# Kernel optimization log

Measured on AMD Instinct MI355X. Metric: run time of the kernel, lower is better.

Reference implementation:

```python
import jax, jax.numpy as jnp
import numpy as np

N = 100000      # nodes
E = 1200000     # edges
B = 128         # graphs
H = 64          # hidden
IN_DIM = 64
GN_EPS = 1e-5


def _gin(x, edge_index, w1, b1, w2, b2):
    # GINConv (eps=0): mlp(x + sum_{j in N(i)} x_j)
    agg = jax.ops.segment_sum(x[edge_index[0]], edge_index[1], num_segments=N)
    h = x + agg
    return jax.nn.relu(h @ w1 + b1) @ w2 + b2


def _graph_norm(x, batch, w, b, ms):
    # PyG GraphNorm: out = w * (x - ms*mean) / sqrt(var + eps) + b, per-graph stats
    ones = jnp.ones((x.shape[0],), x.dtype)
    cnt = jnp.maximum(jax.ops.segment_sum(ones, batch, num_segments=B), 1.0)[:, None]
    mean = jax.ops.segment_sum(x, batch, num_segments=B) / cnt
    out = x - ms * mean[batch]
    var = jax.ops.segment_sum(out * out, batch, num_segments=B) / cnt
    return out * (jax.lax.rsqrt(var + GN_EPS)[batch] * w) + b


def setup_inputs() -> dict:
    key = jax.random.key(0)
    ks = jax.random.split(key, 32)
    inp = {
        'x': jax.random.normal(ks[0], (N, IN_DIM), jnp.float32),
        'edge_index': jax.random.randint(ks[1], (2, E), 0, N, dtype=jnp.int32),
        'batch': jnp.sort(jax.random.randint(ks[2], (N,), 0, B, dtype=jnp.int32)),
        'u': jax.random.normal(ks[3], (B, 3), jnp.float32),
    }
    k = 4
    for i in range(3):
        fin = IN_DIM if i == 0 else H
        inp[f'w{i+1}a'] = jax.random.normal(ks[k], (fin, H), jnp.float32) / np.sqrt(fin); k += 1
        inp[f'b{i+1}a'] = jnp.zeros((H,), jnp.float32)
        inp[f'w{i+1}b'] = jax.random.normal(ks[k], (H, H), jnp.float32) / np.sqrt(H); k += 1
        inp[f'b{i+1}b'] = jnp.zeros((H,), jnp.float32)
        inp[f'gn{i+1}_w'] = jnp.ones((H,), jnp.float32)
        inp[f'gn{i+1}_b'] = jnp.zeros((H,), jnp.float32)
        inp[f'gn{i+1}_ms'] = jnp.ones((H,), jnp.float32)
    inp['gate_w'] = jax.random.normal(ks[k], (H, 1), jnp.float32) / np.sqrt(H); k += 1
    inp['gate_b'] = jnp.zeros((1,), jnp.float32)
    inp['hw1'] = jax.random.normal(ks[k], (3 * H + 3, H), jnp.float32) / np.sqrt(3 * H + 3); k += 1
    inp['hb1'] = jnp.zeros((H,), jnp.float32)
    inp['hw2'] = jax.random.normal(ks[k], (H, 1), jnp.float32) / np.sqrt(H); k += 1
    inp['hb2'] = jnp.zeros((1,), jnp.float32)
    return inp


def reference(x, edge_index, batch, u,
              w1a, b1a, w1b, b1b, gn1_w, gn1_b, gn1_ms,
              w2a, b2a, w2b, b2b, gn2_w, gn2_b, gn2_ms,
              w3a, b3a, w3b, b3b, gn3_w, gn3_b, gn3_ms,
              gate_w, gate_b, hw1, hb1, hw2, hb2):
    h1 = jax.nn.relu(_graph_norm(_gin(x, edge_index, w1a, b1a, w1b, b1b), batch, gn1_w, gn1_b, gn1_ms))
    h2 = jax.nn.relu(_graph_norm(_gin(h1, edge_index, w2a, b2a, w2b, b2b), batch, gn2_w, gn2_b, gn2_ms))
    h3 = jax.nn.relu(_graph_norm(_gin(h2, edge_index, w3a, b3a, w3b, b3b), batch, gn3_w, gn3_b, gn3_ms))
    h = h1 + h2 + h3

    # AttentionalAggregation: per-graph softmax over gate logits
    gate = h @ gate_w + gate_b                                      # [N,1]
    m = jax.ops.segment_max(gate, batch, num_segments=B)            # [B,1]
    ex = jnp.exp(gate - m[batch])
    den = jax.ops.segment_sum(ex, batch, num_segments=B)
    att = jax.ops.segment_sum((ex / den[batch]) * h, batch, num_segments=B)

    ones = jnp.ones((h.shape[0],), h.dtype)
    cnt = jnp.maximum(jax.ops.segment_sum(ones, batch, num_segments=B), 1.0)[:, None]
    mean_pool = jax.ops.segment_sum(h, batch, num_segments=B) / cnt
    max_pool = jax.ops.segment_max(h, batch, num_segments=B)

    z = jnp.concatenate([att, mean_pool, max_pool, u], axis=1)       # [B, 3H+3]
    out = jax.nn.relu(z @ hw1 + hb1) @ hw2 + hb2                     # head_cls
    return out.reshape(-1)
```

## Files before the change

kernel.cpp:

```cpp
#include <hip/hip_runtime.h>
#include <hip/hip_cooperative_groups.h>
#include <math.h>

namespace cg = cooperative_groups;

#define HDIM 64
#define GN_EPS 1e-5f
#define MAXNB 512
#define APITCH 72
#define RCHUNK 8192

typedef __attribute__((ext_vector_type(8))) short bf16x8;
typedef __attribute__((ext_vector_type(4))) float f32x4;

__device__ __forceinline__ int lower_bound_i(const int* a, int n, int key){
  int lo = 0, hi = n;
  while (lo < hi){ int mid = (lo + hi) >> 1; if (a[mid] < key) lo = mid + 1; else hi = mid; }
  return lo;
}
__device__ __forceinline__ unsigned fenc(float x){
  unsigned b = __float_as_uint(x);
  return (b & 0x80000000u) ? ~b : (b | 0x80000000u);
}
__device__ __forceinline__ float fdec(unsigned u){
  unsigned b = (u & 0x80000000u) ? (u ^ 0x80000000u) : ~u;
  return __uint_as_float(b);
}
__device__ __forceinline__ unsigned short f2bf(float f){
  unsigned u = __float_as_uint(f);
  u += 0x7fffu + ((u >> 16) & 1u);
  return (unsigned short)(u >> 16);
}
__device__ __forceinline__ float bf2f(unsigned short h){
  return __uint_as_float(((unsigned)h) << 16);
}
__device__ __forceinline__ void addbf(float* a, uint4 v){
  a[0] += __uint_as_float(v.x << 16);
  a[1] += __uint_as_float(v.x & 0xffff0000u);
  a[2] += __uint_as_float(v.y << 16);
  a[3] += __uint_as_float(v.y & 0xffff0000u);
  a[4] += __uint_as_float(v.z << 16);
  a[5] += __uint_as_float(v.z & 0xffff0000u);
  a[6] += __uint_as_float(v.w << 16);
  a[7] += __uint_as_float(v.w & 0xffff0000u);
}

struct BuildArgs {
  const int* src; const int* dst; int E; int NB;
  const float* W0; const float* W1; const float* W2;
  const float* W3; const float* W4; const float* W5;
  short* wbf;
  const int* batch; int N; int* gs; int B;
  int* bcount; int* bbase; int* bcursor;
  int2* ebuf; int* deg; int* offs; int* csr;
  const float* x; unsigned short* xb; int n16;
  float* stats; int statsN; float* poolz; int poolzN;
};

__global__ void k_build(BuildArgs a){
  cg::grid_group grid = cg::this_grid();
  __shared__ int sA[512];
  __shared__ int sB[512];
  int tid = threadIdx.x;
  int gsz = (int)gridDim.x;
  int gstart = blockIdx.x * 256 + tid;
  int gstride = gsz * 256;

  for (int i = gstart; i <= MAXNB; i += gstride) a.bcount[i] = 0;
  for (int i = gstart; i < a.statsN; i += gstride) a.stats[i] = 0.f;
  for (int i = gstart; i < a.poolzN; i += gstride) a.poolz[i] = 0.f;
  if (blockIdx.x < 6){
    const float* Wsrc = (blockIdx.x == 0) ? a.W0 : (blockIdx.x == 1) ? a.W1 :
                        (blockIdx.x == 2) ? a.W2 : (blockIdx.x == 3) ? a.W3 :
                        (blockIdx.x == 4) ? a.W4 : a.W5;
    short* hi = a.wbf + blockIdx.x * 8192;
    short* lo = hi + 4096;
    for (int i = tid; i < 4096; i += 256){
      int k = i >> 6, j = i & 63;
      float v = Wsrc[i];
      unsigned short h = f2bf(v);
      hi[j * 64 + k] = (short)h;
      lo[j * 64 + k] = (short)f2bf(v - bf2f(h));
    }
  } else if (blockIdx.x == 6){
    for (int g = tid; g <= a.B; g += 256) a.gs[g] = lower_bound_i(a.batch, a.N, g);
  }
  for (int i = gstart; i < a.n16; i += gstride){
    float4 v = ((const float4*)a.x)[i];
    ushort4 o;
    o.x = f2bf(v.x); o.y = f2bf(v.y); o.z = f2bf(v.z); o.w = f2bf(v.w);
    ((ushort4*)a.xb)[i] = o;
  }
  grid.sync();

  for (int b = tid; b < a.NB; b += 256) sA[b] = 0;
  __syncthreads();
  for (int i = gstart; i < a.E; i += gstride) atomicAdd(&sA[a.dst[i] >> 8], 1);
  __syncthreads();
  for (int b = tid; b < a.NB; b += 256){ int c = sA[b]; if (c) atomicAdd(&a.bcount[b], c); }
  grid.sync();

  if (blockIdx.x == 0){
    int v0 = (2 * tid     < a.NB) ? a.bcount[2 * tid]     : 0;
    int v1 = (2 * tid + 1 < a.NB) ? a.bcount[2 * tid + 1] : 0;
    int L = v0 + v1;
    sB[tid] = L; __syncthreads();
    for (int o = 1; o < 256; o <<= 1){
      int tv = (tid >= o) ? sB[tid - o] : 0;
      __syncthreads();
      sB[tid] += tv;
      __syncthreads();
    }
    int run = sB[tid] - L;
    if (2 * tid < a.NB){ a.bbase[2 * tid] = run; a.bcursor[2 * tid] = run; }
    run += v0;
    if (2 * tid + 1 < a.NB){ a.bbase[2 * tid + 1] = run; a.bcursor[2 * tid + 1] = run; }
    if (tid == 255) a.bbase[a.NB] = sB[255];
  }
  grid.sync();

  int nch = (a.E + RCHUNK - 1) / RCHUNK;
  for (int ci = blockIdx.x; ci < nch; ci += gsz){
    int c0 = ci * RCHUNK;
    for (int b = tid; b < a.NB; b += 256) sA[b] = 0;
    __syncthreads();
    for (int j = 0; j < RCHUNK / 256; j++){
      int i = c0 + j * 256 + tid;
      if (i < a.E) atomicAdd(&sA[a.dst[i] >> 8], 1);
    }
    __syncthreads();
    for (int b = tid; b < a.NB; b += 256){
      int c = sA[b];
      sB[b] = c ? atomicAdd(&a.bcursor[b], c) : 0;
      sA[b] = 0;
    }
    __syncthreads();
    for (int j = 0; j < RCHUNK / 256; j++){
      int i = c0 + j * 256 + tid;
      if (i < a.E){
        int d = a.dst[i]; int b = d >> 8;
        int rr = atomicAdd(&sA[b], 1);
        a.ebuf[sB[b] + rr] = make_int2(a.src[i], d);
      }
    }
    __syncthreads();
  }
  grid.sync();

  for (int b = blockIdx.x; b < a.NB; b += gsz){
    int lo = b << 8;
    int nn = min(256, a.N - lo);
    sA[tid] = 0; __syncthreads();
    int es = a.bbase[b], ee = a.bbase[b + 1];
    for (int i = es + tid; i < ee; i += 256) atomicAdd(&sA[a.ebuf[i].y - lo], 1);
    __syncthreads();
    int v = sA[tid];
    sB[tid] = v; __syncthreads();
    for (int o = 1; o < 256; o <<= 1){
      int tv = (tid >= o) ? sB[tid - o] : 0;
      __syncthreads();
      sB[tid] += tv;
      __syncthreads();
    }
    int excl = sB[tid] - v;
    if (tid < nn){ a.deg[lo + tid] = v; a.offs[lo + tid] = es + excl; }
    __syncthreads();
    sA[tid] = es + excl;
    __syncthreads();
    for (int i = es + tid; i < ee; i += 256){
      int2 e = a.ebuf[i];
      int pos = atomicAdd(&sA[e.y - lo], 1);
      a.csr[pos] = e.x;
    }
    __syncthreads();
  }
}

struct TrunkArgs {
  const unsigned short* xb;
  unsigned short* bufA; unsigned short* bufB;
  float* G; float* hsum;
  const int* csr; const int* offs; const int* deg; const int* batch; const int* gs;
  const short* wbf;
  const float* B1a; const float* B1b; const float* B1c;
  const float* B2a; const float* B2b; const float* B2c;
  const float* gnw0; const float* gnw1; const float* gnw2;
  const float* gnb0; const float* gnb1; const float* gnb2;
  const float* gnm0; const float* gnm1; const float* gnm2;
  float* stats; int N; int n16; int B;
  const float* gw; const float* gb; const float* u;
  const float* hw1; const float* hb1; const float* hw2; const float* hb2;
  float* sumbuf; unsigned* maxbuf; float* attbuf; float* denbuf; unsigned* gmaxbuf;
  float* gatebuf; float* out;
};

__global__ __launch_bounds__(256, 3) void k_trunk(TrunkArgs a){
  cg::grid_group grid = cg::this_grid();
  __shared__ __align__(16) char smem[51712];
  short* Ws  = (short*)smem;
  short* Ah  = (short*)(smem + 32768);
  short* Al  = (short*)(smem + 32768 + 9216);
  float* ssum = (float*)(smem + 32768 + 18432);
  float* ssq  = ssum + 64;
  int tid = threadIdx.x;
  int wv = tid >> 6, lane = tid & 63;
  int gsz = (int)gridDim.x;
  int N = a.N;
  int ntile = (N + 63) >> 6;

  const unsigned short* P = a.xb;
  unsigned short* Cb = a.bufA;

  for (int l = 0; l < 3; l++){
    {
      int sub = lane >> 3, l8 = lane & 7, sbase = sub << 3;
      const uint4* Pv = (const uint4*)P;
      int wid = blockIdx.x * 4 + wv;
      int wstep = gsz * 4 * 8;
      for (int nb = wid * 8; nb < N; nb += wstep){
        int node = nb + sub;
        bool ok = node < N;
        int st = 0, cnt = 0;
        if (ok){ st = a.offs[node]; cnt = a.deg[node]; }
        float acc8[8];
        #pragma unroll
        for (int k = 0; k < 8; k++) acc8[k] = 0.f;
        if (ok) addbf(acc8, Pv[(size_t)node * 8 + l8]);
        for (int base = 0; base < cnt; base += 8){
          int rem = cnt - base;
          int s = (l8 < rem) ? a.csr[st + base + l8] : 0;
          int m = min(rem, 8);
          int j = 0;
          for (; j + 4 <= m; j += 4){
            int s0 = __shfl(s, sbase | j);
            int s1 = __shfl(s, sbase | (j + 1));
            int s2 = __shfl(s, sbase | (j + 2));
            int s3 = __shfl(s, sbase | (j + 3));
            uint4 v0 = Pv[(size_t)s0 * 8 + l8];
            uint4 v1 = Pv[(size_t)s1 * 8 + l8];
            uint4 v2 = Pv[(size_t)s2 * 8 + l8];
            uint4 v3 = Pv[(size_t)s3 * 8 + l8];
            addbf(acc8, v0); addbf(acc8, v1); addbf(acc8, v2); addbf(acc8, v3);
          }
          for (; j < m; ++j){
            int sj = __shfl(s, sbase | j);
            addbf(acc8, Pv[(size_t)sj * 8 + l8]);
          }
        }
        if (ok){
          float4* Gp = (float4*)(a.G + (size_t)node * HDIM + l8 * 8);
          Gp[0] = make_float4(acc8[0], acc8[1], acc8[2], acc8[3]);
          Gp[1] = make_float4(acc8[4], acc8[5], acc8[6], acc8[7]);
        }
      }
    }
    grid.sync();

    {
      const short* Wall = a.wbf + (size_t)l * 16384;
      for (int j = tid; j < 2048; j += 256){
        int p = j >> 9, rem = j & 511, rr = rem >> 3, c8 = rem & 7;
        bf16x8 v = ((const bf16x8*)Wall)[j];
        *(bf16x8*)(Ws + p * 4096 + rr * 64 + ((c8 ^ (rr & 7)) << 3)) = v;
      }
      int quad = lane >> 4, l15 = lane & 15;
      int rbase = wv << 4;
      int h7 = l15 & 7;
      const float* B1 = (l == 0) ? a.B1a : (l == 1) ? a.B1b : a.B1c;
      const float* B2 = (l == 0) ? a.B2a : (l == 1) ? a.B2b : a.B2c;
      float bb1[4], bb2[4];
      #pragma unroll
      for (int t4 = 0; t4 < 4; t4++){ bb1[t4] = B1[t4 * 16 + l15]; bb2[t4] = B2[t4 * 16 + l15]; }
      float* lstats = a.stats + (size_t)l * a.B * 128;

      int t = blockIdx.x;
      float4 r[4], r2[4];
      #pragma unroll
      for (int ri = 0; ri < 4; ri++){ r[ri] = make_float4(0.f,0.f,0.f,0.f); r2[ri] = r[ri]; }
      if (t < ntile){
        int tb = t << 6;
        #pragma unroll
        for (int ri = 0; ri < 4; ri++){
          int idx = ri * 256 + tid;
          int node = tb + (idx >> 4), f4 = idx & 15;
          if (node < N) r[ri] = ((const float4*)a.G)[(size_t)node * 16 + f4];
        }
      }
      while (t < ntile){
        int t0 = t << 6;
        #pragma unroll
        for (int ri = 0; ri < 4; ri++){
          int idx = ri * 256 + tid;
          int nodeL = idx >> 4, f4 = idx & 15;
          float vv[4] = {r[ri].x, r[ri].y, r[ri].z, r[ri].w};
          short hh[4], ll[4];
          #pragma unroll
          for (int j = 0; j < 4; j++){
            unsigned short hv = f2bf(vv[j]);
            hh[j] = (short)hv;
            ll[j] = (short)f2bf(vv[j] - bf2f(hv));
          }
          *(short4*)(Ah + nodeL * APITCH + f4 * 4) = make_short4(hh[0], hh[1], hh[2], hh[3]);
          *(short4*)(Al + nodeL * APITCH + f4 * 4) = make_short4(ll[0], ll[1], ll[2], ll[3]);
        }
        if (tid < 64){ ssum[tid] = 0.f; ssq[tid] = 0.f; }
        __syncthreads();

        int tn = t + gsz;
        #pragma unroll
        for (int ri = 0; ri < 4; ri++) r2[ri] = make_float4(0.f,0.f,0.f,0.f);
        if (tn < ntile){
          int tb = tn << 6;
          #pragma unroll
          for (int ri = 0; ri < 4; ri++){
            int idx = ri * 256 + tid;
            int node = tb + (idx >> 4), f4 = idx & 15;
            if (node < N) r2[ri] = ((const float4*)a.G)[(size_t)node * 16 + f4];
          }
        }

        f32x4 acc[4];
        #pragma unroll
        for (int t4 = 0; t4 < 4; t4++) acc[t4] = (f32x4){0.f, 0.f, 0.f, 0.f};
        #pragma unroll
        for (int kb = 0; kb < 2; kb++){
          int kk = kb * 32 + quad * 8;
          int swz = ((kb * 4 + quad) ^ h7) << 3;
          bf16x8 a_h = *(const bf16x8*)(Ah + (rbase + l15) * APITCH + kk);
          bf16x8 a_l = *(const bf16x8*)(Al + (rbase + l15) * APITCH + kk);
          #pragma unroll
          for (int t4 = 0; t4 < 4; t4++){
            int row = t4 * 16 + l15;
            bf16x8 b_h = *(const bf16x8*)(Ws + row * 64 + swz);
            bf16x8 b_l = *(const bf16x8*)(Ws + 4096 + row * 64 + swz);
            acc[t4] = __builtin_amdgcn_mfma_f32_16x16x32_bf16(a_h, b_h, acc[t4], 0, 0, 0);
            acc[t4] = __builtin_amdgcn_mfma_f32_16x16x32_bf16(a_h, b_l, acc[t4], 0, 0, 0);
            acc[t4] = __builtin_amdgcn_mfma_f32_16x16x32_bf16(a_l, b_h, acc[t4], 0, 0, 0);
          }
        }
        __syncthreads();

        #pragma unroll
        for (int t4 = 0; t4 < 4; t4++){
          #pragma unroll
          for (int rg = 0; rg < 4; rg++){
            float v = fmaxf(acc[t4][rg] + bb1[t4], 0.f);
            int row = rbase + quad * 4 + rg;
            int col = t4 * 16 + l15;
            unsigned short hv = f2bf(v);
            Ah[row * APITCH + col] = (short)hv;
            Al[row * APITCH + col] = (short)f2bf(v - bf2f(hv));
          }
        }
        __syncthreads();

        f32x4 acc2[4];
        #pragma unroll
        for (int t4 = 0; t4 < 4; t4++) acc2[t4] = (f32x4){0.f, 0.f, 0.f, 0.f};
        #pragma unroll
        for (int kb = 0; kb < 2; kb++){
          int kk = kb * 32 + quad * 8;
          int swz = ((kb * 4 + quad) ^ h7) << 3;
          bf16x8 a_h = *(const bf16x8*)(Ah + (rbase + l15) * APITCH + kk);
          bf16x8 a_l = *(const bf16x8*)(Al + (rbase + l15) * APITCH + kk);
          #pragma unroll
          for (int t4 = 0; t4 < 4; t4++){
            int row = t4 * 16 + l15;
            bf16x8 b_h = *(const bf16x8*)(Ws + 8192 + row * 64 + swz);
            bf16x8 b_l = *(const bf16x8*)(Ws + 12288 + row * 64 + swz);
            acc2[t4] = __builtin_amdgcn_mfma_f32_16x16x32_bf16(a_h, b_h, acc2[t4], 0, 0, 0);
            acc2[t4] = __builtin_amdgcn_mfma_f32_16x16x32_bf16(a_h, b_l, acc2[t4], 0, 0, 0);
            acc2[t4] = __builtin_amdgcn_mfma_f32_16x16x32_bf16(a_l, b_h, acc2[t4], 0, 0, 0);
          }
        }

        int lastn = min(t0 + 63, N - 1);
        int g0 = a.batch[t0];
        bool uniform = (a.batch[lastn] == g0) && (t0 + 63 < N);
        #pragma unroll
        for (int t4 = 0; t4 < 4; t4++){
          int f = t4 * 16 + l15;
          float s = 0.f, q = 0.f;
          #pragma unroll
          for (int rg = 0; rg < 4; rg++){
            float v = acc2[t4][rg] + bb2[t4];
            int node = t0 + rbase + quad * 4 + rg;
            if (node < N) a.G[(size_t)node * HDIM + f] = v;
            if (uniform){
              s += v; q += v * v;
            } else if (node < N){
              int g = a.batch[node];
              atomicAdd(&lstats[g * 128 + f], v);
              atomicAdd(&lstats[g * 128 + 64 + f], v * v);
            }
          }
          if (uniform){
            s += __shfl_xor(s, 16); s += __shfl_xor(s, 32);
            q += __shfl_xor(q, 16); q += __shfl_xor(q, 32);
            if (quad == 0){ atomicAdd(&ssum[f], s); atomicAdd(&ssq[f], q); }
          }
        }
        __syncthreads();
        if (uniform && tid < 64){
          atomicAdd(&lstats[g0 * 128 + tid], ssum[tid]);
          atomicAdd(&lstats[g0 * 128 + 64 + tid], ssq[tid]);
        }
        #pragma unroll
        for (int ri = 0; ri < 4; ri++) r[ri] = r2[ri];
        t = tn;
      }
    }
    grid.sync();

    {
      const float* wv_ = (l == 0) ? a.gnw0 : (l == 1) ? a.gnw1 : a.gnw2;
      const float* bv_ = (l == 0) ? a.gnb0 : (l == 1) ? a.gnb1 : a.gnb2;
      const float* mv_ = (l == 0) ? a.gnm0 : (l == 1) ? a.gnm1 : a.gnm2;
      const float* lstats = a.stats + (size_t)l * a.B * 128;
      int first = (l == 0) ? 1 : 0;
      int writeC = (l == 2) ? 0 : 1;
      for (int i = blockIdx.x * 256 + tid; i < a.n16; i += gsz * 256){
        int node = i >> 4, q = i & 15;
        int g = a.batch[node];
        float cnt = (float)max(a.gs[g + 1] - a.gs[g], 1);
        float4 y  = ((const float4*)a.G)[i];
        float4 s1 = ((const float4*)(lstats + g * 128))[q];
        float4 s2 = ((const float4*)(lstats + g * 128 + 64))[q];
        float4 wq = ((const float4*)wv_)[q];
        float4 mq = ((const float4*)mv_)[q];
        float4 bq = ((const float4*)bv_)[q];
        float4 v;
        #define APPLY1(c) { \
          float mean = s1.c / cnt; float ex2 = s2.c / cnt; \
          float var = ex2 - (2.f * mq.c - mq.c * mq.c) * mean * mean; \
          float sc = rsqrtf(var + GN_EPS) * wq.c; \
          v.c = fmaxf((y.c - mq.c * mean) * sc + bq.c, 0.f); }
        APPLY1(x) APPLY1(y) APPLY1(z) APPLY1(w)
        #undef APPLY1
        if (writeC){
          ushort4 o;
          o.x = f2bf(v.x); o.y = f2bf(v.y); o.z = f2bf(v.z); o.w = f2bf(v.w);
          ((ushort4*)Cb)[i] = o;
        }
        if (first){
          ((float4*)a.hsum)[i] = v;
        } else {
          float4 h = ((float4*)a.hsum)[i];
          h.x += v.x; h.y += v.y; h.z += v.z; h.w += v.w;
          ((float4*)a.hsum)[i] = h;
        }
      }
    }
    grid.sync();
    P = Cb;
    Cb = (l == 0) ? a.bufB : a.bufA;
  }

  {
    int nchunk = (N + 31) >> 5;
    int wid = blockIdx.x * 4 + wv;
    float gwv = a.gw[lane];
    float gb = a.gb[0];
    for (int c = wid; c < nchunk; c += gsz * 4){
      int s = c << 5, e = min(s + 32, N);
      int cur = a.batch[s];
      float macc = 0.f, xacc = -INFINITY, gmx = -INFINITY;
      for (int nd = s; nd < e; ++nd){
        int g = a.batch[nd];
        if (g != cur){
          atomicAdd(&a.sumbuf[cur * 64 + lane], macc);
          atomicMax(&a.maxbuf[cur * 64 + lane], fenc(xacc));
          if (lane == 0) atomicMax(&a.gmaxbuf[cur], fenc(gmx));
          macc = 0.f; xacc = -INFINITY; gmx = -INFINITY; cur = g;
        }
        float hv = a.hsum[(size_t)nd * HDIM + lane];
        macc += hv; xacc = fmaxf(xacc, hv);
        float gv = hv * gwv;
        #pragma unroll
        for (int msk = 1; msk < 64; msk <<= 1) gv += __shfl_xor(gv, msk);
        gv += gb;
        if (lane == 0) a.gatebuf[nd] = gv;
        gmx = fmaxf(gmx, gv);
      }
      atomicAdd(&a.sumbuf[cur * 64 + lane], macc);
      atomicMax(&a.maxbuf[cur * 64 + lane], fenc(xacc));
      if (lane == 0) atomicMax(&a.gmaxbuf[cur], fenc(gmx));
    }
  }
  grid.sync();

  {
    int nchunk = (N + 31) >> 5;
    int wid = blockIdx.x * 4 + wv;
    for (int c = wid; c < nchunk; c += gsz * 4){
      int s = c << 5, e = min(s + 32, N);
      int cur = a.batch[s];
      float m = fdec(a.gmaxbuf[cur]);
      float aacc = 0.f, dacc = 0.f;
      for (int nd = s; nd < e; ++nd){
        int g = a.batch[nd];
        if (g != cur){
          atomicAdd(&a.attbuf[cur * 64 + lane], aacc);
          if (lane == 0) atomicAdd(&a.denbuf[cur], dacc);
          aacc = 0.f; dacc = 0.f; cur = g; m = fdec(a.gmaxbuf[cur]);
        }
        float ex = expf(a.gatebuf[nd] - m);
        float hv = a.hsum[(size_t)nd * HDIM + lane];
        aacc += ex * hv; dacc += ex;
      }
      atomicAdd(&a.attbuf[cur * 64 + lane], aacc);
      if (lane == 0) atomicAdd(&a.denbuf[cur], dacc);
    }
  }
  grid.sync();

  {
    float* z = (float*)smem;
    int g = blockIdx.x;
    if (g < a.B){
      float cnt = (float)max(a.gs[g + 1] - a.gs[g], 1);
      if (tid < 64){
        float den = a.denbuf[g];
        z[tid]       = a.attbuf[g * 64 + tid] / den;
        z[64 + tid]  = a.sumbuf[g * 64 + tid] / cnt;
        z[128 + tid] = fdec(a.maxbuf[g * 64 + tid]);
        if (tid < 3) z[192 + tid] = a.u[g * 3 + tid];
      }
      __syncthreads();
      if (tid < 64){
        float acc = a.hb1[tid];
        for (int k = 0; k < 195; k++) acc += z[k] * a.hw1[k * 64 + tid];
        float sv = fmaxf(acc, 0.f) * a.hw2[tid];
        #pragma unroll
        for (int msk = 1; msk < 64; msk <<= 1) sv += __shfl_xor(sv, msk);
        if (tid == 0) a.out[g] = sv + a.hb2[0];
      }
    }
  }
}

__global__ void k_prep(const int* __restrict__ dst, int* __restrict__ bcount, int E, int NB,
                       const float* __restrict__ Wa0, const float* __restrict__ Wb0,
                       const float* __restrict__ Wa1, const float* __restrict__ Wb1,
                       const float* __restrict__ Wa2, const float* __restrict__ Wb2,
                       short* __restrict__ wbf,
                       const int* __restrict__ batch, int N, int* __restrict__ gs, int B){
  int tid = threadIdx.x;
  if (blockIdx.x < 256){
    __shared__ int lh[MAXNB];
    for (int b = tid; b < NB; b += 256) lh[b] = 0;
    __syncthreads();
    for (int i = blockIdx.x * 256 + tid; i < E; i += 256 * 256)
      atomicAdd(&lh[dst[i] >> 8], 1);
    __syncthreads();
    for (int b = tid; b < NB; b += 256){ int c = lh[b]; if (c) atomicAdd(&bcount[b], c); }
  } else if (blockIdx.x < 262){
    int wi = blockIdx.x - 256;
    const float* Wsrc[6] = {Wa0, Wb0, Wa1, Wb1, Wa2, Wb2};
    const float* W = Wsrc[wi];
    short* hi = wbf + wi * 8192;
    short* lo = hi + 4096;
    for (int i = tid; i < 4096; i += 256){
      int k = i >> 6, j = i & 63;
      float v = W[i];
      unsigned short h = f2bf(v);
      hi[j * 64 + k] = (short)h;
      lo[j * 64 + k] = (short)f2bf(v - bf2f(h));
    }
  } else {
    for (int g = tid; g <= B; g += 256) gs[g] = lower_bound_i(batch, N, g);
  }
}

__global__ void k_cvt(const float* __restrict__ x, unsigned short* __restrict__ xb, int n16){
  int i = blockIdx.x * blockDim.x + threadIdx.x;
  if (i >= n16) return;
  float4 v = ((const float4*)x)[i];
  ushort4 o;
  o.x = f2bf(v.x); o.y = f2bf(v.y); o.z = f2bf(v.z); o.w = f2bf(v.w);
  ((ushort4*)xb)[i] = o;
}

__global__ void k_bscan(const int* __restrict__ bcount, int* __restrict__ bbase,
                        int* __restrict__ bcursor, int NB){
  __shared__ int sd[MAXNB];
  int tid = threadIdx.x;
  int v = (tid < NB) ? bcount[tid] : 0;
  sd[tid] = v; __syncthreads();
  for (int o = 1; o < MAXNB; o <<= 1){
    int t = (tid >= o) ? sd[tid - o] : 0;
    __syncthreads();
    sd[tid] += t;
    __syncthreads();
  }
  int excl = sd[tid] - v;
  if (tid < NB){ bbase[tid] = excl; bcursor[tid] = excl; }
  if (tid == NB - 1) bbase[NB] = excl + v;
}

__global__ void k_breorder(const int* __restrict__ src, const int* __restrict__ dst,
                           int* __restrict__ bcursor, int2* __restrict__ ebuf, int E, int NB){
  __shared__ int lh[MAXNB];
  __shared__ int lbase[MAXNB];
  int tid = threadIdx.x;
  int c0 = blockIdx.x * RCHUNK;
  for (int b = tid; b < NB; b += 256) lh[b] = 0;
  __syncthreads();
  for (int j = 0; j < RCHUNK / 256; j++){
    int i = c0 + j * 256 + tid;
    if (i < E) atomicAdd(&lh[dst[i] >> 8], 1);
  }
  __syncthreads();
  for (int b = tid; b < NB; b += 256){
    int c = lh[b];
    lbase[b] = c ? atomicAdd(&bcursor[b], c) : 0;
    lh[b] = 0;
  }
  __syncthreads();
  for (int j = 0; j < RCHUNK / 256; j++){
    int i = c0 + j * 256 + tid;
    if (i < E){
      int d = dst[i]; int b = d >> 8;
      int r = atomicAdd(&lh[b], 1);
      ebuf[lbase[b] + r] = make_int2(src[i], d);
    }
  }
}

__global__ void k_bucket_csr(const int2* __restrict__ ebuf, const int* __restrict__ bbase,
                             int* __restrict__ deg, int* __restrict__ offs,
                             int* __restrict__ csr, int N){
  __shared__ int lh[256];
  __shared__ int lsc[256];
  int b = blockIdx.x;
  int lo = b << 8;
  int nn = min(256, N - lo);
  int tid = threadIdx.x;
  lh[tid] = 0; __syncthreads();
  int es = bbase[b], ee = bbase[b + 1];
  for (int i = es + tid; i < ee; i += 256) atomicAdd(&lh[ebuf[i].y - lo], 1);
  __syncthreads();
  int v = lh[tid];
  lsc[tid] = v; __syncthreads();
  for (int o = 1; o < 256; o <<= 1){
    int t = (tid >= o) ? lsc[tid - o] : 0;
    __syncthreads();
    lsc[tid] += t;
    __syncthreads();
  }
  int excl = lsc[tid] - v;
  if (tid < nn){ deg[lo + tid] = v; offs[lo + tid] = es + excl; }
  __syncthreads();
  lh[tid] = es + excl;
  __syncthreads();
  for (int i = es + tid; i < ee; i += 256){
    int2 e = ebuf[i];
    int pos = atomicAdd(&lh[e.y - lo], 1);
    csr[pos] = e.x;
  }
}

__global__ __launch_bounds__(256) void k_agg(
    const unsigned short* __restrict__ Pb, const int* __restrict__ csr,
    const int* __restrict__ offs, const int* __restrict__ deg,
    float* __restrict__ G, int n){
  int tid = threadIdx.x;
  int wave_id = blockIdx.x * 4 + (tid >> 6);
  int lane = tid & 63;
  int sub = lane >> 3, l8 = lane & 7;
  int node = wave_id * 8 + sub;
  bool ok = node < n;
  int st = 0, cnt = 0;
  if (ok){ st = offs[node]; cnt = deg[node]; }
  const uint4* Pv = (const uint4*)Pb;
  float a[8];
  #pragma unroll
  for (int k = 0; k < 8; k++) a[k] = 0.f;
  if (ok) addbf(a, Pv[(size_t)node * 8 + l8]);
  int sbase = sub << 3;
  for (int base = 0; base < cnt; base += 8){
    int rem = cnt - base;
    int s = (l8 < rem) ? csr[st + base + l8] : 0;
    int m = min(rem, 8);
    int j = 0;
    for (; j + 4 <= m; j += 4){
      int s0 = __shfl(s, sbase | j);
      int s1 = __shfl(s, sbase | (j + 1));
      int s2 = __shfl(s, sbase | (j + 2));
      int s3 = __shfl(s, sbase | (j + 3));
      uint4 v0 = Pv[(size_t)s0 * 8 + l8];
      uint4 v1 = Pv[(size_t)s1 * 8 + l8];
      uint4 v2 = Pv[(size_t)s2 * 8 + l8];
      uint4 v3 = Pv[(size_t)s3 * 8 + l8];
      addbf(a, v0); addbf(a, v1); addbf(a, v2); addbf(a, v3);
    }
    for (; j < m; ++j){
      int sj = __shfl(s, sbase | j);
      addbf(a, Pv[(size_t)sj * 8 + l8]);
    }
  }
  if (ok){
    float4* Gp = (float4*)(G + (size_t)node * HDIM + l8 * 8);
    Gp[0] = make_float4(a[0], a[1], a[2], a[3]);
    Gp[1] = make_float4(a[4], a[5], a[6], a[7]);
  }
}

__global__ __launch_bounds__(256, 3) void k_mlp(
    float* __restrict__ G, const int* __restrict__ batch,
    const short* __restrict__ Wall,
    const float* __restrict__ B1, const float* __restrict__ B2,
    float* __restrict__ stats, int N){
  __shared__ short Ws[16384];
  __shared__ short Ah[64 * APITCH];
  __shared__ short Al[64 * APITCH];
  __shared__ float ssum[64], ssq[64];
  int tid = threadIdx.x;

  for (int j = tid; j < 2048; j += 256){
    int p = j >> 9, rem = j & 511, rr = rem >> 3, c8 = rem & 7;
    bf16x8 v = ((const bf16x8*)Wall)[j];
    *(bf16x8*)(Ws + p * 4096 + rr * 64 + ((c8 ^ (rr & 7)) << 3)) = v;
  }

  int wv = tid >> 6, lane = tid & 63;
  int quad = lane >> 4, l15 = lane & 15;
  int rbase = wv << 4;
  int h7 = l15 & 7;
  float bb1[4], bb2[4];
  #pragma unroll
  for (int t = 0; t < 4; t++){ bb1[t] = B1[t * 16 + l15]; bb2[t] = B2[t * 16 + l15]; }

  int tile0 = blockIdx.x << 1;
  float4 r[4], r2[4];
  {
    int tb = tile0 << 6;
    #pragma unroll
    for (int ri = 0; ri < 4; ri++){
      int idx = ri * 256 + tid;
      int node = tb + (idx >> 4), f4 = idx & 15;
      r[ri] = make_float4(0.f, 0.f, 0.f, 0.f);
      if (node < N) r[ri] = ((const float4*)G)[(size_t)node * 16 + f4];
    }
  }

  for (int tt = 0; tt < 2; tt++){
    int t0 = (tile0 + tt) << 6;
    if (t0 >= N) break;

    #pragma unroll
    for (int ri = 0; ri < 4; ri++){
      int idx = ri * 256 + tid;
      int node = idx >> 4, f4 = idx & 15;
      float vv[4] = {r[ri].x, r[ri].y, r[ri].z, r[ri].w};
      short h[4], l[4];
      #pragma unroll
      for (int j = 0; j < 4; j++){
        unsigned short hh = f2bf(vv[j]);
        h[j] = (short)hh;
        l[j] = (short)f2bf(vv[j] - bf2f(hh));
      }
      *(short4*)(Ah + node * APITCH + f4 * 4) = make_short4(h[0], h[1], h[2], h[3]);
      *(short4*)(Al + node * APITCH + f4 * 4) = make_short4(l[0], l[1], l[2], l[3]);
    }
    if (tid < 64){ ssum[tid] = 0.f; ssq[tid] = 0.f; }
    __syncthreads();

    if (tt == 0){
      int tb = (tile0 + 1) << 6;
      #pragma unroll
      for (int ri = 0; ri < 4; ri++){
        int idx = ri * 256 + tid;
        int node = tb + (idx >> 4), f4 = idx & 15;
        r2[ri] = make_float4(0.f, 0.f, 0.f, 0.f);
        if (node < N) r2[ri] = ((const float4*)G)[(size_t)node * 16 + f4];
      }
    }

    f32x4 acc[4];
    #pragma unroll
    for (int t = 0; t < 4; t++) acc[t] = (f32x4){0.f, 0.f, 0.f, 0.f};
    #pragma unroll
    for (int kb = 0; kb < 2; kb++){
      int kk = kb * 32 + quad * 8;
      int swz = ((kb * 4 + quad) ^ h7) << 3;
      bf16x8 a_h = *(const bf16x8*)(Ah + (rbase + l15) * APITCH + kk);
      bf16x8 a_l = *(const bf16x8*)(Al + (rbase + l15) * APITCH + kk);
      #pragma unroll
      for (int t = 0; t < 4; t++){
        int row = t * 16 + l15;
        bf16x8 b_h = *(const bf16x8*)(Ws + row * 64 + swz);
        bf16x8 b_l = *(const bf16x8*)(Ws + 4096 + row * 64 + swz);
        acc[t] = __builtin_amdgcn_mfma_f32_16x16x32_bf16(a_h, b_h, acc[t], 0, 0, 0);
        acc[t] = __builtin_amdgcn_mfma_f32_16x16x32_bf16(a_h, b_l, acc[t], 0, 0, 0);
        acc[t] = __builtin_amdgcn_mfma_f32_16x16x32_bf16(a_l, b_h, acc[t], 0, 0, 0);
      }
    }
    __syncthreads();

    #pragma unroll
    for (int t = 0; t < 4; t++){
      #pragma unroll
      for (int rg = 0; rg < 4; rg++){
        float v = fmaxf(acc[t][rg] + bb1[t], 0.f);
        int row = rbase + quad * 4 + rg;
        int col = t * 16 + l15;
        unsigned short hh = f2bf(v);
        Ah[row * APITCH + col] = (short)hh;
        Al[row * APITCH + col] = (short)f2bf(v - bf2f(hh));
      }
    }
    __syncthreads();

    f32x4 acc2[4];
    #pragma unroll
    for (int t = 0; t < 4; t++) acc2[t] = (f32x4){0.f, 0.f, 0.f, 0.f};
    #pragma unroll
    for (int kb = 0; kb < 2; kb++){
      int kk = kb * 32 + quad * 8;
      int swz = ((kb * 4 + quad) ^ h7) << 3;
      bf16x8 a_h = *(const bf16x8*)(Ah + (rbase + l15) * APITCH + kk);
      bf16x8 a_l = *(const bf16x8*)(Al + (rbase + l15) * APITCH + kk);
      #pragma unroll
      for (int t = 0; t < 4; t++){
        int row = t * 16 + l15;
        bf16x8 b_h = *(const bf16x8*)(Ws + 8192 + row * 64 + swz);
        bf16x8 b_l = *(const bf16x8*)(Ws + 12288 + row * 64 + swz);
        acc2[t] = __builtin_amdgcn_mfma_f32_16x16x32_bf16(a_h, b_h, acc2[t], 0, 0, 0);
        acc2[t] = __builtin_amdgcn_mfma_f32_16x16x32_bf16(a_h, b_l, acc2[t], 0, 0, 0);
        acc2[t] = __builtin_amdgcn_mfma_f32_16x16x32_bf16(a_l, b_h, acc2[t], 0, 0, 0);
      }
    }

    int lastn = min(t0 + 63, N - 1);
    int g0 = batch[t0];
    bool uniform = (batch[lastn] == g0) && (t0 + 63 < N);
    #pragma unroll
    for (int t = 0; t < 4; t++){
      int f = t * 16 + l15;
      float s = 0.f, q = 0.f;
      #pragma unroll
      for (int rg = 0; rg < 4; rg++){
        float v = acc2[t][rg] + bb2[t];
        int node = t0 + rbase + quad * 4 + rg;
        if (node < N) G[(size_t)node * HDIM + f] = v;
        if (uniform){
          s += v; q += v * v;
        } else if (node < N){
          int g = batch[node];
          atomicAdd(&stats[g * 128 + f], v);
          atomicAdd(&stats[g * 128 + 64 + f], v * v);
        }
      }
      if (uniform){
        s += __shfl_xor(s, 16); s += __shfl_xor(s, 32);
        q += __shfl_xor(q, 16); q += __shfl_xor(q, 32);
        if (quad == 0){ atomicAdd(&ssum[f], s); atomicAdd(&ssq[f], q); }
      }
    }
    __syncthreads();
    if (uniform && tid < 64){
      atomicAdd(&stats[g0 * 128 + tid], ssum[tid]);
      atomicAdd(&stats[g0 * 128 + 64 + tid], ssq[tid]);
    }
    #pragma unroll
    for (int ri = 0; ri < 4; ri++) r[ri] = r2[ri];
  }
}

__global__ void k_gn_apply(const float* __restrict__ Y, const int* __restrict__ batch,
                           const float* __restrict__ stats, const int* __restrict__ gs,
                           const float* __restrict__ w, const float* __restrict__ ms,
                           const float* __restrict__ bias,
                           unsigned short* __restrict__ Cb, float* __restrict__ hsum, int n16,
                           int first, int writeC){
  int i = blockIdx.x * blockDim.x + threadIdx.x;
  if (i >= n16) return;
  int node = i >> 4, q = i & 15;
  int g = batch[node];
  float cnt = (float)max(gs[g + 1] - gs[g], 1);
  float4 y  = ((const float4*)Y)[i];
  float4 s1 = ((const float4*)(stats + g * 128))[q];
  float4 s2 = ((const float4*)(stats + g * 128 + 64))[q];
  float4 wv = ((const float4*)w)[q];
  float4 mv = ((const float4*)ms)[q];
  float4 bv = ((const float4*)bias)[q];
  float4 v;
  #define APPLY1(c) { \
    float mean = s1.c / cnt; float ex2 = s2.c / cnt; \
    float var = ex2 - (2.f * mv.c - mv.c * mv.c) * mean * mean; \
    float sc = rsqrtf(var + GN_EPS) * wv.c; \
    v.c = fmaxf((y.c - mv.c * mean) * sc + bv.c, 0.f); }
  APPLY1(x) APPLY1(y) APPLY1(z) APPLY1(w)
  #undef APPLY1
  if (writeC){
    ushort4 o;
    o.x = f2bf(v.x); o.y = f2bf(v.y); o.z = f2bf(v.z); o.w = f2bf(v.w);
    ((ushort4*)Cb)[i] = o;
  }
  if (first){
    ((float4*)hsum)[i] = v;
  } else {
    float4 h = ((float4*)hsum)[i];
    h.x += v.x; h.y += v.y; h.z += v.z; h.w += v.w;
    ((float4*)hsum)[i] = h;
  }
}

#define GN_NPW 32
__global__ void k_pool1(const float* __restrict__ HS, const int* __restrict__ batch,
                        const float* __restrict__ GW, const float* __restrict__ GB,
                        float* __restrict__ sumbuf, unsigned* __restrict__ maxbuf,
                        float* __restrict__ gatebuf, unsigned* __restrict__ gmaxbuf, int n){
  int wave = (int)((blockIdx.x * blockDim.x + threadIdx.x) >> 6);
  int lane = threadIdx.x & 63;
  int s = wave * GN_NPW;
  if (s >= n) return;
  int e = min(s + GN_NPW, n);
  float gwv = GW[lane];
  float gb = GB[0];
  int cur = batch[s];
  float macc = 0.f, xacc = -INFINITY, gmx = -INFINITY;
  for (int nd = s; nd < e; ++nd){
    int g = batch[nd];
    if (g != cur){
      atomicAdd(&sumbuf[cur * 64 + lane], macc);
      atomicMax(&maxbuf[cur * 64 + lane], fenc(xacc));
      if (lane == 0) atomicMax(&gmaxbuf[cur], fenc(gmx));
      macc = 0.f; xacc = -INFINITY; gmx = -INFINITY; cur = g;
    }
    float hv = HS[(size_t)nd * HDIM + lane];
    macc += hv; xacc = fmaxf(xacc, hv);
    float gv = hv * gwv;
    #pragma unroll
    for (int msk = 1; msk < 64; msk <<= 1) gv += __shfl_xor(gv, msk);
    gv += gb;
    if (lane == 0) gatebuf[nd] = gv;
    gmx = fmaxf(gmx, gv);
  }
  atomicAdd(&sumbuf[cur * 64 + lane], macc);
  atomicMax(&maxbuf[cur * 64 + lane], fenc(xacc));
  if (lane == 0) atomicMax(&gmaxbuf[cur], fenc(gmx));
}

__global__ void k_pool2(const float* __restrict__ HS, const int* __restrict__ batch,
                        const float* __restrict__ gatebuf, const unsigned* __restrict__ gmaxbuf,
                        float* __restrict__ attbuf, float* __restrict__ denbuf, int n){
  int wave = (int)((blockIdx.x * blockDim.x + threadIdx.x) >> 6);
  int lane = threadIdx.x & 63;
  int s = wave * GN_NPW;
  if (s >= n) return;
  int e = min(s + GN_NPW, n);
  int cur = batch[s];
  float m = fdec(gmaxbuf[cur]);
  float aacc = 0.f, dacc = 0.f;
  for (int nd = s; nd < e; ++nd){
    int g = batch[nd];
    if (g != cur){
      atomicAdd(&attbuf[cur * 64 + lane], aacc);
      if (lane == 0) atomicAdd(&denbuf[cur], dacc);
      aacc = 0.f; dacc = 0.f; cur = g; m = fdec(gmaxbuf[cur]);
    }
    float ex = expf(gatebuf[nd] - m);
    float hv = HS[(size_t)nd * HDIM + lane];
    aacc += ex * hv; dacc += ex;
  }
  atomicAdd(&attbuf[cur * 64 + lane], aacc);
  if (lane == 0) atomicAdd(&denbuf[cur], dacc);
}

__global__ void k_pool3(const float* __restrict__ attbuf, const float* __restrict__ denbuf,
                        const float* __restrict__ sumbuf, const unsigned* __restrict__ maxbuf,
                        const int* __restrict__ gs, const float* __restrict__ U,
                        const float* __restrict__ HW1, const float* __restrict__ HB1,
                        const float* __restrict__ HW2, const float* __restrict__ HB2,
                        float* __restrict__ out){
  __shared__ float z[200];
  int g = blockIdx.x;
  int tid = threadIdx.x;
  float cnt = (float)max(gs[g + 1] - gs[g], 1);
  float den = denbuf[g];
  z[tid]       = attbuf[g * 64 + tid] / den;
  z[64 + tid]  = sumbuf[g * 64 + tid] / cnt;
  z[128 + tid] = fdec(maxbuf[g * 64 + tid]);
  if (tid < 3) z[192 + tid] = U[g * 3 + tid];
  __syncthreads();
  float acc = HB1[tid];
  for (int k = 0; k < 195; k++) acc += z[k] * HW1[k * 64 + tid];
  float sv = fmaxf(acc, 0.f) * HW2[tid];
  #pragma unroll
  for (int msk = 1; msk < 64; msk <<= 1) sv += __shfl_xor(sv, msk);
  if (tid == 0) out[g] = sv + HB2[0];
}

extern "C" void kernel_launch(void* const* d_in, const int* in_sizes, int n_in,
                              void* d_out, int out_size, void* d_ws, size_t ws_size,
                              hipStream_t stream){
  const float* x     = (const float*)d_in[0];
  const int*   ei    = (const int*)d_in[1];
  const int*   batch = (const int*)d_in[2];
  const float* u     = (const float*)d_in[3];
  const float* W[3][4]; const float* GNp[3][3];
  for (int l = 0; l < 3; l++){
    int base = 4 + l * 7;
    W[l][0]  = (const float*)d_in[base + 0];
    W[l][1]  = (const float*)d_in[base + 1];
    W[l][2]  = (const float*)d_in[base + 2];
    W[l][3]  = (const float*)d_in[base + 3];
    GNp[l][0]= (const float*)d_in[base + 4];
    GNp[l][1]= (const float*)d_in[base + 5];
    GNp[l][2]= (const float*)d_in[base + 6];
  }
  const float* gate_w = (const float*)d_in[25];
  const float* gate_b = (const float*)d_in[26];
  const float* hw1    = (const float*)d_in[27];
  const float* hb1    = (const float*)d_in[28];
  const float* hw2    = (const float*)d_in[29];
  const float* hb2    = (const float*)d_in[30];
  float* out = (float*)d_out;

  int N = in_sizes[0] / HDIM;
  int E = in_sizes[1] / 2;
  int B = in_sizes[3] / 3;
  const int* src = ei;
  const int* dst = ei + E;
  int NB = (N + 255) >> 8;
  int n16 = N * 16;

  char* w8 = (char*)d_ws;
  size_t NH = (size_t)N * HDIM * sizeof(float);
  size_t NHb = (size_t)N * HDIM * sizeof(short);
  auto alignup = [](size_t v){ return (v + 255) & ~(size_t)255; };
  size_t off = 0;
  float* hsum    = (float*)(w8 + off); off += alignup(NH);
  float* G       = (float*)(w8 + off); off += alignup(NH);
  unsigned short* xb   = (unsigned short*)(w8 + off); off += alignup(NHb);
  unsigned short* bufA = (unsigned short*)(w8 + off); off += alignup(NHb);
  unsigned short* bufB = (unsigned short*)(w8 + off); off += alignup(NHb);
  float* gatebuf = (float*)(w8 + off); off += alignup((size_t)N * 4);
  int*   deg     = (int*)(w8 + off);   off += alignup((size_t)N * 4);
  int*   offs    = (int*)(w8 + off);   off += alignup((size_t)N * 4);
  int*   csr     = (int*)(w8 + off);   off += alignup((size_t)E * 4);
  int2*  ebuf    = (int2*)(w8 + off);  off += alignup((size_t)E * 8);
  int*   bcount  = (int*)(w8 + off);   off += alignup((size_t)(MAXNB + 1) * 4);
  int*   bbase   = (int*)(w8 + off);   off += alignup((size_t)(MAXNB + 1) * 4);
  int*   bcursor = (int*)(w8 + off);   off += alignup((size_t)(MAXNB + 1) * 4);
  float* stats   = (float*)(w8 + off); off += alignup((size_t)3 * B * 128 * 4);
  float* poolz   = (float*)(w8 + off);
  int poolzN = B * 64 * 3 + 2 * B;
  off += alignup((size_t)poolzN * 4);
  float*    sumbuf  = poolz;
  unsigned* maxbuf  = (unsigned*)(poolz + (size_t)B * 64);
  float*    attbuf  = poolz + (size_t)2 * B * 64;
  float*    denbuf  = poolz + (size_t)3 * B * 64;
  unsigned* gmaxbuf = (unsigned*)(poolz + (size_t)3 * B * 64 + B);
  int*   gs      = (int*)(w8 + off);   off += alignup((size_t)(B + 1) * 4);
  short* wbf     = (short*)(w8 + off); off += alignup((size_t)6 * 8192 * 2);
  (void)ws_size; (void)n_in; (void)out_size;

  int dev = 0; hipGetDevice(&dev);
  int coopAttr = 0, nCU = 0;
  hipDeviceGetAttribute(&coopAttr, hipDeviceAttributeCooperativeLaunch, dev);
  hipDeviceGetAttribute(&nCU, hipDeviceAttributeMultiprocessorCount, dev);
  int mbB = 0, mbT = 0;
  hipOccupancyMaxActiveBlocksPerMultiprocessor(&mbB, k_build, 256, 0);
  hipOccupancyMaxActiveBlocksPerMultiprocessor(&mbT, k_trunk, 256, 0);
  bool coop = coopAttr && nCU > 0 && mbB >= 1 && mbT >= 3 &&
              (long)mbT * nCU >= (long)B && (long)mbB * nCU >= 8;

  bool done = false;
  if (coop){
    BuildArgs ba;
    ba.src = src; ba.dst = dst; ba.E = E; ba.NB = NB;
    ba.W0 = W[0][0]; ba.W1 = W[0][2]; ba.W2 = W[1][0];
    ba.W3 = W[1][2]; ba.W4 = W[2][0]; ba.W5 = W[2][2];
    ba.wbf = wbf;
    ba.batch = batch; ba.N = N; ba.gs = gs; ba.B = B;
    ba.bcount = bcount; ba.bbase = bbase; ba.bcursor = bcursor;
    ba.ebuf = ebuf; ba.deg = deg; ba.offs = offs; ba.csr = csr;
    ba.x = x; ba.xb = xb; ba.n16 = n16;
    ba.stats = stats; ba.statsN = 3 * B * 128; ba.poolz = poolz; ba.poolzN = poolzN;

    TrunkArgs ta;
    ta.xb = xb; ta.bufA = bufA; ta.bufB = bufB; ta.G = G; ta.hsum = hsum;
    ta.csr = csr; ta.offs = offs; ta.deg = deg; ta.batch = batch; ta.gs = gs;
    ta.wbf = wbf;
    ta.B1a = W[0][1]; ta.B1b = W[1][1]; ta.B1c = W[2][1];
    ta.B2a = W[0][3]; ta.B2b = W[1][3]; ta.B2c = W[2][3];
    ta.gnw0 = GNp[0][0]; ta.gnw1 = GNp[1][0]; ta.gnw2 = GNp[2][0];
    ta.gnb0 = GNp[0][1]; ta.gnb1 = GNp[1][1]; ta.gnb2 = GNp[2][1];
    ta.gnm0 = GNp[0][2]; ta.gnm1 = GNp[1][2]; ta.gnm2 = GNp[2][2];
    ta.stats = stats; ta.N = N; ta.n16 = n16; ta.B = B;
    ta.gw = gate_w; ta.gb = gate_b; ta.u = u;
    ta.hw1 = hw1; ta.hb1 = hb1; ta.hw2 = hw2; ta.hb2 = hb2;
    ta.sumbuf = sumbuf; ta.maxbuf = maxbuf; ta.attbuf = attbuf;
    ta.denbuf = denbuf; ta.gmaxbuf = gmaxbuf;
    ta.gatebuf = gatebuf; ta.out = out;

    int gridB = mbB * nCU; if (gridB > 1024) gridB = 1024;
    int gridT = mbT * nCU; if (gridT > 1024) gridT = 1024;
    void* bp[] = { &ba };
    void* tp[] = { &ta };
    hipError_t e = hipLaunchCooperativeKernel((const void*)k_build, dim3(gridB), dim3(256),
                                              bp, 0, stream);
    if (e == hipSuccess)
      e = hipLaunchCooperativeKernel((const void*)k_trunk, dim3(gridT), dim3(256),
                                     tp, 0, stream);
    done = (e == hipSuccess);
  }

  if (!done){
    hipMemsetAsync(stats, 0, (size_t)3 * B * 128 * 4, stream);
    hipMemsetAsync(poolz, 0, (size_t)poolzN * 4, stream);
    hipMemsetAsync(bcount, 0, (size_t)(MAXNB + 1) * 4, stream);

    const int tb = 256;
    k_prep<<<263, tb, 0, stream>>>(dst, bcount, E, NB,
                                   W[0][0], W[0][2], W[1][0], W[1][2], W[2][0], W[2][2],
                                   wbf, batch, N, gs, B);
    k_cvt<<<(n16 + tb - 1) / tb, tb, 0, stream>>>(x, xb, n16);
    k_bscan<<<1, MAXNB, 0, stream>>>(bcount, bbase, bcursor, NB);
    k_breorder<<<(E + RCHUNK - 1) / RCHUNK, tb, 0, stream>>>(src, dst, bcursor, ebuf, E, NB);
    k_bucket_csr<<<NB, tb, 0, stream>>>(ebuf, bbase, deg, offs, csr, N);

    int nwaves = (N + GN_NPW - 1) / GN_NPW;
    int segblocks = (nwaves * 64 + tb - 1) / tb;
    int nblk64 = (N + 63) >> 6;
    int nblk2 = (nblk64 + 1) >> 1;
    int aggwaves = (N + 7) >> 3;
    int aggblocks = (aggwaves + 3) >> 2;

    const unsigned short* P = xb;
    unsigned short* C = bufA;
    for (int l = 0; l < 3; l++){
      k_agg<<<aggblocks, 256, 0, stream>>>(P, csr, offs, deg, G, N);
      float* lstats = stats + (size_t)l * B * 128;
      k_mlp<<<nblk2, 256, 0, stream>>>(G, batch, wbf + (size_t)l * 16384,
                                       W[l][1], W[l][3], lstats, N);
      k_gn_apply<<<(n16 + tb - 1) / tb, tb, 0, stream>>>(G, batch, lstats, gs,
                                                         GNp[l][0], GNp[l][2], GNp[l][1],
                                                         C, hsum, n16, l == 0 ? 1 : 0,
                                                         l == 2 ? 0 : 1);
      P = C;
      C = (l == 0) ? bufB : bufA;
    }
    k_pool1<<<segblocks, tb, 0, stream>>>(hsum, batch, gate_w, gate_b,
                                          sumbuf, maxbuf, gatebuf, gmaxbuf, N);
    k_pool2<<<segblocks, tb, 0, stream>>>(hsum, batch, gatebuf, gmaxbuf, attbuf, denbuf, N);
    k_pool3<<<B, 64, 0, stream>>>(attbuf, denbuf, sumbuf, maxbuf, gs, u,
                                  hw1, hb1, hw2, hb2, out);
  }
}
```

Before: 486.8 us.

## Assign each block a contiguous node range across all trunk phases

Replaces grid-stride loops in the cooperative trunk kernel with a static contiguous partition of 64-node tiles per block, used consistently by the aggregation, MLP, GraphNorm apply and pooling phases. Each block now touches the same node range in every phase, which can improve L2 locality of the bufA/G/hsum rows it wrote earlier. Contiguous ranges also make the batch-sorted segments within a block more uniform, so fewer atomics are needed. The cost is possible load imbalance, since blocks no longer interleave work and the per-block tile count may differ by one.

After: 493.6 us. About the same (+1.4%).

```diff
diff --git a/kernel.cpp b/kernel.cpp
--- a/kernel.cpp
+++ b/kernel.cpp
@@ -208,6 +208,11 @@
   int N = a.N;
   int ntile = (N + 63) >> 6;
 
+  int ts = (int)(((long)ntile * blockIdx.x) / gsz);
+  int te = (int)(((long)ntile * (blockIdx.x + 1)) / gsz);
+  int ns = ts << 6;
+  int ne = min(te << 6, N);
+
   const unsigned short* P = a.xb;
   unsigned short* Cb = a.bufA;
 
@@ -215,11 +220,9 @@
     {
       int sub = lane >> 3, l8 = lane & 7, sbase = sub << 3;
       const uint4* Pv = (const uint4*)P;
-      int wid = blockIdx.x * 4 + wv;
-      int wstep = gsz * 4 * 8;
-      for (int nb = wid * 8; nb < N; nb += wstep){
+      for (int nb = ns + wv * 8; nb < ne; nb += 32){
         int node = nb + sub;
-        bool ok = node < N;
+        bool ok = node < ne;
         int st = 0, cnt = 0;
         if (ok){ st = a.offs[node]; cnt = a.deg[node]; }
         float acc8[8];
@@ -273,11 +276,11 @@
       for (int t4 = 0; t4 < 4; t4++){ bb1[t4] = B1[t4 * 16 + l15]; bb2[t4] = B2[t4 * 16 + l15]; }
       float* lstats = a.stats + (size_t)l * a.B * 128;
 
-      int t = blockIdx.x;
+      int t = ts;
       float4 r[4], r2[4];
       #pragma unroll
       for (int ri = 0; ri < 4; ri++){ r[ri] = make_float4(0.f,0.f,0.f,0.f); r2[ri] = r[ri]; }
-      if (t < ntile){
+      if (t < te){
         int tb = t << 6;
         #pragma unroll
         for (int ri = 0; ri < 4; ri++){
@@ -286,7 +289,7 @@
           if (node < N) r[ri] = ((const float4*)a.G)[(size_t)node * 16 + f4];
         }
       }
-      while (t < ntile){
+      while (t < te){
         int t0 = t << 6;
         #pragma unroll
         for (int ri = 0; ri < 4; ri++){
@@ -306,10 +309,10 @@
         if (tid < 64){ ssum[tid] = 0.f; ssq[tid] = 0.f; }
         __syncthreads();
 
-        int tn = t + gsz;
+        int tn = t + 1;
         #pragma unroll
         for (int ri = 0; ri < 4; ri++) r2[ri] = make_float4(0.f,0.f,0.f,0.f);
-        if (tn < ntile){
+        if (tn < te){
           int tb = tn << 6;
           #pragma unroll
           for (int ri = 0; ri < 4; ri++){
@@ -419,7 +422,9 @@
       const float* lstats = a.stats + (size_t)l * a.B * 128;
       int first = (l == 0) ? 1 : 0;
       int writeC = (l == 2) ? 0 : 1;
-      for (int i = blockIdx.x * 256 + tid; i < a.n16; i += gsz * 256){
+      int i0 = ts << 10;
+      int i1 = min(te << 10, a.n16);
+      for (int i = i0 + tid; i < i1; i += 256){
         int node = i >> 4, q = i & 15;
         int g = a.batch[node];
         float cnt = (float)max(a.gs[g + 1] - a.gs[g], 1);
@@ -458,10 +463,10 @@
 
   {
     int nchunk = (N + 31) >> 5;
-    int wid = blockIdx.x * 4 + wv;
+    int c0 = ts * 2, c1 = min(te * 2, nchunk);
     float gwv = a.gw[lane];
     float gb = a.gb[0];
-    for (int c = wid; c < nchunk; c += gsz * 4){
+    for (int c = c0 + wv; c < c1; c += 4){
       int s = c << 5, e = min(s + 32, N);
       int cur = a.batch[s];
       float macc = 0.f, xacc = -INFINITY, gmx = -INFINITY;
@@ -491,8 +496,8 @@
 
   {
     int nchunk = (N + 31) >> 5;
-    int wid = blockIdx.x * 4 + wv;
-    for (int c = wid; c < nchunk; c += gsz * 4){
+    int c0 = ts * 2, c1 = min(te * 2, nchunk);
+    for (int c = c0 + wv; c < c1; c += 4){
       int s = c << 5, e = min(s + 32, N);
       int cur = a.batch[s];
       float m = fdec(a.gmaxbuf[cur]);
```
